# Kernel optimization log

Hardware: AMD Instinct MI355X
Metric: run time of the kernel (lower is better)

The kernel has to match this reference:

```python
import jax, jax.numpy as jnp
import numpy as np

_CLIP_MIN = 1e-06
_POS_ALPHA = 0.001
NUM_CLASSES = 26
RADIUS = 3
POOL = 3  # rmi_pool_size == rmi_pool_stride
HALF_D = RADIUS * RADIUS


def _max_pool2d(x):
    # torch F.max_pool2d(kernel=3, stride=3, padding=1): pads with -inf
    return jax.lax.reduce_window(
        x, -jnp.inf, jax.lax.max,
        window_dimensions=(1, 1, POOL, POOL),
        window_strides=(1, 1, POOL, POOL),
        padding=[(0, 0), (0, 0), (1, 1), (1, 1)])


def _get_pairs(x):
    # stack radius^2 shifted views: [n,c,H,W] -> [n,c,half_d,new_h,new_w]
    h, w = x.shape[2], x.shape[3]
    nh, nw = h - (RADIUS - 1), w - (RADIUS - 1)
    views = [x[:, :, y:y + nh, xx:xx + nw] for y in range(RADIUS) for xx in range(RADIUS)]
    return jnp.stack(views, axis=2)


def _log_det_by_cholesky(m):
    chol = jnp.linalg.cholesky(m)
    diag = jnp.diagonal(chol, axis1=-2, axis2=-1)
    return 2.0 * jnp.sum(jnp.log(diag + 1e-08), axis=-1)


def _rmi_lower_bound(labels_4D, probs_4D):
    labels_4D = _max_pool2d(labels_4D)
    probs_4D = _max_pool2d(probs_4D)
    n, c = labels_4D.shape[0], labels_4D.shape[1]
    la = _get_pairs(labels_4D).reshape(n, c, HALF_D, -1)  # [n,c,9,M]
    pr = _get_pairs(probs_4D).reshape(n, c, HALF_D, -1)
    eye = jnp.eye(HALF_D, dtype=pr.dtype)
    la = la - jnp.mean(la, axis=3, keepdims=True)
    pr = pr - jnp.mean(pr, axis=3, keepdims=True)
    la_cov = jnp.einsum('ncdm,ncem->ncde', la, la)
    pr_cov = jnp.einsum('ncdm,ncem->ncde', pr, pr)
    pr_cov_inv = jnp.linalg.inv(pr_cov + eye * _POS_ALPHA)
    la_pr_cov = jnp.einsum('ncdm,ncem->ncde', la, pr)
    appro_var = la_cov - jnp.einsum('ncde,ncef,ncgf->ncdg', la_pr_cov, pr_cov_inv, la_pr_cov)
    rmi_now = 0.5 * _log_det_by_cholesky(appro_var + eye * _POS_ALPHA)  # [n,c]
    rmi_per_class = jnp.mean(rmi_now.reshape(-1, NUM_CLASSES), axis=0) / float(HALF_D)
    return jnp.sum(rmi_per_class)


def setup_inputs() -> dict:
    key = jax.random.key(0)
    k1, k2, k3 = jax.random.split(key, 3)
    n, c, h, w = 4, NUM_CLASSES, 512, 512
    cls_score = jax.random.normal(k1, (n, c, h, w), dtype=jnp.float32)
    new_targets = jax.random.randint(k2, (n, c, h, w), 0, 2).astype(jnp.float32)
    valid_indices = jax.random.randint(k3, (n, h, w), 0, 2).astype(jnp.float32)
    return {"cls_score": cls_score, "new_targets": new_targets, "valid_indices": valid_indices}


def reference(cls_score, new_targets, valid_indices):
    mask = valid_indices[:, None, :, :]  # [n,1,h,w]
    valid_onehot = new_targets * mask
    probs = jax.nn.sigmoid(cls_score) * mask + _CLIP_MIN
    return _rmi_lower_bound(valid_onehot, probs)
```

## Files before the change

### kernel.cpp

```cpp
#include <hip/hip_runtime.h>
#include <math.h>

#define NUM_CLASSES 26
#define HH 512
#define WW 512
#define NB 4
#define PHH 171
#define PWW 171
#define NHH 169
#define NWW 169
#define MPTS (NHH*NWW)
#define NCT (NB*NUM_CLASSES)
#define CLIPV 1e-6f
#define NCHUNK 8
#define RPC 22
#define NSLOT 189

__global__ __launch_bounds__(256, 3) void fused_kernel(const float* __restrict__ cls,
        const float* __restrict__ tgt, const float* __restrict__ mask,
        float* __restrict__ partial) {
    const int nc = blockIdx.x, ch = blockIdx.y;
    const int n = nc / NUM_CLASSES;
    const int lane = threadIdx.x & 63, wave = threadIdx.x >> 6;
    const int rowbase = ch * RPC;
    const int rc = (rowbase + RPC <= NHH) ? RPC : (NHH - rowbase);
    const int trows = rc + 2;

    __shared__ float tP[24][176];
    __shared__ float tL[24][176];
    __shared__ float amS[4][512];
    __shared__ float lmS[4][512];

    const float4* c4 = (const float4*)(cls  + (size_t)nc * HH * WW);
    const float4* t4 = (const float4*)(tgt  + (size_t)nc * HH * WW);
    const float4* m4 = (const float4*)(mask + (size_t)n  * HH * WW);

    for (int k = 0; k < 6; ++k) {
        int tr = wave + 4 * k;
        if (tr >= trows) break;
        int ph = rowbase + tr;
        float am[8], lm[8];
        #pragma unroll
        for (int j = 0; j < 8; ++j) { am[j] = -INFINITY; lm[j] = 0.f; }
        const int r0 = 3 * ph - 1;
        #pragma unroll
        for (int s = 0; s < 3; ++s) {
            int r = r0 + s;
            r = r < 0 ? 0 : r;
            int rb = r * 128;
            #pragma unroll
            for (int g = 0; g < 2; ++g) {
                int i4 = rb + lane + 64 * g;
                float4 c = c4[i4];
                float4 t = t4[i4];
                float4 m = m4[i4];
                float cc[4] = {c.x, c.y, c.z, c.w};
                float tt[4] = {t.x, t.y, t.z, t.w};
                float mm[4] = {m.x, m.y, m.z, m.w};
                #pragma unroll
                for (int q = 0; q < 4; ++q) {
                    int j = 4 * g + q;
                    am[j] = fmaxf(am[j], mm[q] > 0.5f ? cc[q] : -INFINITY);
                    lm[j] = fmaxf(lm[j], tt[q] * mm[q]);
                }
            }
        }
        *(float4*)&amS[wave][4 * lane]       = make_float4(am[0], am[1], am[2], am[3]);
        *(float4*)&amS[wave][256 + 4 * lane] = make_float4(am[4], am[5], am[6], am[7]);
        *(float4*)&lmS[wave][4 * lane]       = make_float4(lm[0], lm[1], lm[2], lm[3]);
        *(float4*)&lmS[wave][256 + 4 * lane] = make_float4(lm[4], lm[5], lm[6], lm[7]);
        #pragma unroll
        for (int j = 0; j < 3; ++j) {
            int pw = lane + 64 * j;
            if (pw < PWW) {
                int cM = 3 * pw;
                float a = fmaxf(amS[wave][cM], amS[wave][cM + 1]);
                float l = fmaxf(lmS[wave][cM], lmS[wave][cM + 1]);
                if (cM > 0) {
                    a = fmaxf(a, amS[wave][cM - 1]);
                    l = fmaxf(l, lmS[wave][cM - 1]);
                }
                tP[tr][pw] = __fdividef(1.0f, 1.0f + __expf(-a)) + CLIPV;
                tL[tr][pw] = (l > 0.5f) ? 1.0f : 0.0f;
            }
        }
        if (lane < 5) {
            tP[tr][171 + lane] = 0.f;
            tL[tr][171 + lane] = 0.f;
        }
    }
    __syncthreads();

    const int items = rc * 43;
    float* pbase = partial + (size_t)ch * NSLOT * NCT + nc;

    if (wave < 2) {
        const float (*src)[176] = wave ? tP : tL;
        float acc[45], sm[9];
        #pragma unroll
        for (int k = 0; k < 45; ++k) acc[k] = 0.f;
        #pragma unroll
        for (int k = 0; k < 9; ++k) sm[k] = 0.f;

        for (int it = lane; it < items; it += 64) {
            int tr = it / 43;
            int j0 = (it - tr * 43) * 4;
            const float* rp = &src[tr][j0];
            float4 x0 = *(const float4*)(rp);
            float4 x1 = *(const float4*)(rp + 4);
            float4 y0 = *(const float4*)(rp + 176);
            float4 y1 = *(const float4*)(rp + 180);
            float4 z0 = *(const float4*)(rp + 352);
            float4 z1 = *(const float4*)(rp + 356);
            float r0[8] = {x0.x, x0.y, x0.z, x0.w, x1.x, x1.y, x1.z, x1.w};
            float r1[8] = {y0.x, y0.y, y0.z, y0.w, y1.x, y1.y, y1.z, y1.w};
            float r2[8] = {z0.x, z0.y, z0.z, z0.w, z1.x, z1.y, z1.z, z1.w};
            #pragma unroll
            for (int q = 0; q < 4; ++q) {
                float sel = (j0 + q < NWW) ? 1.f : 0.f;
                float v[9], vs[9];
                v[0] = r0[q]; v[1] = r0[q + 1]; v[2] = r0[q + 2];
                v[3] = r1[q]; v[4] = r1[q + 1]; v[5] = r1[q + 2];
                v[6] = r2[q]; v[7] = r2[q + 1]; v[8] = r2[q + 2];
                #pragma unroll
                for (int d = 0; d < 9; ++d) { vs[d] = v[d] * sel; sm[d] += vs[d]; }
                int k = 0;
                #pragma unroll
                for (int d = 0; d < 9; ++d)
                    #pragma unroll
                    for (int e = d; e < 9; ++e)
                        acc[k++] += vs[d] * v[e];
            }
        }
        #pragma unroll
        for (int k = 0; k < 45; ++k) {
            float x = acc[k];
            #pragma unroll
            for (int off = 32; off > 0; off >>= 1) x += __shfl_down(x, off);
            if (lane == 0) pbase[(size_t)((wave == 0 ? 0 : 45) + k) * NCT] = x;
        }
        #pragma unroll
        for (int k = 0; k < 9; ++k) {
            float x = sm[k];
            #pragma unroll
            for (int off = 32; off > 0; off >>= 1) x += __shfl_down(x, off);
            if (lane == 0) pbase[(size_t)((wave == 0 ? 171 : 180) + k) * NCT] = x;
        }
    } else {
        const int nd  = (wave == 2) ? 5 : 4;
        const int dof = (wave == 2) ? 0 : 5;
        float acc[45];
        #pragma unroll
        for (int k = 0; k < 45; ++k) acc[k] = 0.f;

        for (int it = lane; it < items; it += 64) {
            int tr = it / 43;
            int j0 = (it - tr * 43) * 4;
            const float* pp = &tP[tr][j0];
            float4 px0 = *(const float4*)(pp);
            float4 px1 = *(const float4*)(pp + 4);
            float4 py0 = *(const float4*)(pp + 176);
            float4 py1 = *(const float4*)(pp + 180);
            float4 pz0 = *(const float4*)(pp + 352);
            float4 pz1 = *(const float4*)(pp + 356);
            float pr0[8] = {px0.x, px0.y, px0.z, px0.w, px1.x, px1.y, px1.z, px1.w};
            float pr1[8] = {py0.x, py0.y, py0.z, py0.w, py1.x, py1.y, py1.z, py1.w};
            float pr2[8] = {pz0.x, pz0.y, pz0.z, pz0.w, pz1.x, pz1.y, pz1.z, pz1.w};
            const float* la  = &tL[tr + (wave == 2 ? 0 : 1)][j0];
            const float* lb2 = &tL[tr + (wave == 2 ? 1 : 2)][j0];
            float4 la0 = *(const float4*)(la);
            float4 la1 = *(const float4*)(la + 4);
            float4 lb0 = *(const float4*)(lb2);
            float4 lb1 = *(const float4*)(lb2 + 4);
            float lrA[8] = {la0.x, la0.y, la0.z, la0.w, la1.x, la1.y, la1.z, la1.w};
            float lrB[8] = {lb0.x, lb0.y, lb0.z, lb0.w, lb1.x, lb1.y, lb1.z, lb1.w};
            #pragma unroll
            for (int q = 0; q < 4; ++q) {
                float sel = (j0 + q < NWW) ? 1.f : 0.f;
                float vp[9];
                vp[0] = pr0[q]; vp[1] = pr0[q + 1]; vp[2] = pr0[q + 2];
                vp[3] = pr1[q]; vp[4] = pr1[q + 1]; vp[5] = pr1[q + 2];
                vp[6] = pr2[q]; vp[7] = pr2[q + 1]; vp[8] = pr2[q + 2];
                float vl[5];
                if (wave == 2) {
                    vl[0] = lrA[q] * sel; vl[1] = lrA[q + 1] * sel; vl[2] = lrA[q + 2] * sel;
                    vl[3] = lrB[q] * sel; vl[4] = lrB[q + 1] * sel;
                } else {
                    vl[0] = lrA[q + 2] * sel;
                    vl[1] = lrB[q] * sel; vl[2] = lrB[q + 1] * sel; vl[3] = lrB[q + 2] * sel;
                }
                #pragma unroll
                for (int d = 0; d < 5; ++d) {
                    if (d < nd) {
                        #pragma unroll
                        for (int e = 0; e < 9; ++e)
                            acc[d * 9 + e] += vl[d] * vp[e];
                    }
                }
            }
        }
        const int nred = nd * 9;
        #pragma unroll
        for (int k = 0; k < 45; ++k) {
            if (k < nred) {
                float x = acc[k];
                #pragma unroll
                for (int off = 32; off > 0; off >>= 1) x += __shfl_down(x, off);
                if (lane == 0) pbase[(size_t)(90 + dof * 9 + k) * NCT] = x;
            }
        }
    }
}

__global__ __launch_bounds__(128) void solve_kernel(const float* __restrict__ partial,
                                                    double* __restrict__ per_nc) {
    const int nc = blockIdx.x;
    const int tid = threadIdx.x;
    __shared__ double cl[45], cp[45], clp[81], sL[9], sP[9];
    __shared__ double All[81], C[81], Pm[81], X[81], A[81];
    __shared__ double logacc;

    for (int s = tid; s < NSLOT; s += 128) {
        double acc = 0.0;
        for (int ch = 0; ch < NCHUNK; ++ch)
            acc += (double)partial[((size_t)ch * NSLOT + s) * NCT + nc];
        if (s < 45)       cl[s] = acc;
        else if (s < 90)  cp[s - 45] = acc;
        else if (s < 171) clp[s - 90] = acc;
        else if (s < 180) sL[s - 171] = acc;
        else              sP[s - 180] = acc;
    }
    if (tid == 0) logacc = 0.0;
    __syncthreads();

    const double M = (double)MPTS;
    if (tid < 81) {
        int d = tid / 9, e = tid % 9;
        int lo = d < e ? d : e, hi = d < e ? e : d;
        int k = 9 * lo - lo * (lo - 1) / 2 + (hi - lo);
        All[tid] = cl[k] - sL[d] * sL[e] / M;
        C[tid]   = cp[k] - sP[d] * sP[e] / M + (d == e ? 1e-3 : 0.0);
        Pm[tid]  = clp[tid] - sL[d] * sP[e] / M;
    }
    __syncthreads();

    for (int k = 0; k < 9; ++k) {
        if (tid == 0) C[k * 9 + k] = sqrt(fmax(C[k * 9 + k], 1e-30));
        __syncthreads();
        if (tid > k && tid < 9) C[tid * 9 + k] /= C[k * 9 + k];
        __syncthreads();
        if (tid < 81) {
            int i = tid / 9, j = tid % 9;
            if (j > k && i >= j) C[i * 9 + j] -= C[i * 9 + k] * C[j * 9 + k];
        }
        __syncthreads();
    }

    for (int e = 0; e < 9; ++e) {
        if (tid < 9) {
            int d = tid;
            double sum = Pm[d * 9 + e];
            for (int k = 0; k < e; ++k) sum -= C[e * 9 + k] * X[k * 9 + d];
            X[e * 9 + d] = sum / C[e * 9 + e];
        }
        __syncthreads();
    }

    if (tid < 81) {
        int d = tid / 9, g = tid % 9;
        double w = 0.0;
        #pragma unroll
        for (int e = 0; e < 9; ++e) w += X[e * 9 + d] * X[e * 9 + g];
        A[tid] = All[tid] - w + (d == g ? 1e-3 : 0.0);
    }
    __syncthreads();

    for (int k = 0; k < 9; ++k) {
        if (tid == 0) {
            double piv = sqrt(fmax(A[k * 9 + k], 0.0));
            A[k * 9 + k] = piv;
            logacc += log(piv + 1e-8);
        }
        __syncthreads();
        if (tid > k && tid < 9) A[tid * 9 + k] /= A[k * 9 + k];
        __syncthreads();
        if (tid < 81) {
            int i = tid / 9, j = tid % 9;
            if (j > k && i >= j) A[i * 9 + j] -= A[i * 9 + k] * A[j * 9 + k];
        }
        __syncthreads();
    }
    if (tid == 0) per_nc[nc] = logacc;
}

__global__ __launch_bounds__(128) void reduce_kernel(const double* __restrict__ per_nc,
                                                     float* __restrict__ out) {
    int t = threadIdx.x;
    double r = (t < NCT) ? per_nc[t] : 0.0;
    __shared__ double red[128];
    red[t] = r;
    __syncthreads();
    for (int s = 64; s > 0; s >>= 1) {
        if (t < s) red[t] += red[t + s];
        __syncthreads();
    }
    if (t == 0) out[0] = (float)(red[0] / 36.0);
}

extern "C" void kernel_launch(void* const* d_in, const int* in_sizes, int n_in,
                              void* d_out, int out_size, void* d_ws, size_t ws_size,
                              hipStream_t stream) {
    const float* cls  = (const float*)d_in[0];
    const float* tgt  = (const float*)d_in[1];
    const float* mask = (const float*)d_in[2];

    double* per_nc  = (double*)d_ws;
    float*  partial = (float*)(per_nc + 128);

    dim3 gfused(NCT, NCHUNK);
    fused_kernel<<<gfused, 256, 0, stream>>>(cls, tgt, mask, partial);

    solve_kernel<<<NCT, 128, 0, stream>>>(partial, per_nc);

    reduce_kernel<<<1, 128, 0, stream>>>(per_nc, (float*)d_out);
}
```

Baseline: 278.0 us.

## Split fused kernel column-wise into two halves to double grid and shrink LDS

```diff
diff --git a/kernel.cpp b/kernel.cpp
--- a/kernel.cpp
+++ b/kernel.cpp
@@ -15,21 +15,29 @@
 #define NCHUNK 8
 #define RPC 22
 #define NSLOT 189
-
-__global__ __launch_bounds__(256, 3) void fused_kernel(const float* __restrict__ cls,
+#define NSLICE (NCHUNK*2)
+#define TW 96
+#define NQ 22
+
+__global__ __launch_bounds__(256, 5) void fused_kernel(const float* __restrict__ cls,
         const float* __restrict__ tgt, const float* __restrict__ mask,
         float* __restrict__ partial) {
-    const int nc = blockIdx.x, ch = blockIdx.y;
+    const int nc = blockIdx.x, ch = blockIdx.y, half = blockIdx.z;
     const int n = nc / NUM_CLASSES;
     const int lane = threadIdx.x & 63, wave = threadIdx.x >> 6;
     const int rowbase = ch * RPC;
     const int rc = (rowbase + RPC <= NHH) ? RPC : (NHH - rowbase);
     const int trows = rc + 2;
 
-    __shared__ float tP[24][176];
-    __shared__ float tL[24][176];
-    __shared__ float amS[4][512];
-    __shared__ float lmS[4][512];
+    const int ibase4 = half ? 65 : 0;
+    const int nf4    = half ? 63 : 72;
+    const int ioff   = half ? 260 : 0;
+    const int cbase  = half ? 88 : 0;
+
+    __shared__ float tP[24][TW];
+    __shared__ float tL[24][TW];
+    __shared__ float amS[4][288];
+    __shared__ float lmS[4][288];
 
     const float4* c4 = (const float4*)(cls  + (size_t)nc * HH * WW);
     const float4* t4 = (const float4*)(tgt  + (size_t)nc * HH * WW);
@@ -50,52 +58,61 @@
             int rb = r * 128;
             #pragma unroll
             for (int g = 0; g < 2; ++g) {
-                int i4 = rb + lane + 64 * g;
-                float4 c = c4[i4];
-                float4 t = t4[i4];
-                float4 m = m4[i4];
-                float cc[4] = {c.x, c.y, c.z, c.w};
-                float tt[4] = {t.x, t.y, t.z, t.w};
-                float mm[4] = {m.x, m.y, m.z, m.w};
-                #pragma unroll
-                for (int q = 0; q < 4; ++q) {
-                    int j = 4 * g + q;
-                    am[j] = fmaxf(am[j], mm[q] > 0.5f ? cc[q] : -INFINITY);
-                    lm[j] = fmaxf(lm[j], tt[q] * mm[q]);
+                int idx = 64 * g + lane;
+                if (idx < nf4) {
+                    int i4 = rb + ibase4 + idx;
+                    float4 c = c4[i4];
+                    float4 t = t4[i4];
+                    float4 m = m4[i4];
+                    float cc[4] = {c.x, c.y, c.z, c.w};
+                    float tt[4] = {t.x, t.y, t.z, t.w};
+                    float mm[4] = {m.x, m.y, m.z, m.w};
+                    #pragma unroll
+                    for (int q = 0; q < 4; ++q) {
+                        int j = 4 * g + q;
+                        am[j] = fmaxf(am[j], mm[q] > 0.5f ? cc[q] : -INFINITY);
+                        lm[j] = fmaxf(lm[j], tt[q] * mm[q]);
+                    }
                 }
             }
         }
-        *(float4*)&amS[wave][4 * lane]       = make_float4(am[0], am[1], am[2], am[3]);
-        *(float4*)&amS[wave][256 + 4 * lane] = make_float4(am[4], am[5], am[6], am[7]);
-        *(float4*)&lmS[wave][4 * lane]       = make_float4(lm[0], lm[1], lm[2], lm[3]);
-        *(float4*)&lmS[wave][256 + 4 * lane] = make_float4(lm[4], lm[5], lm[6], lm[7]);
-        #pragma unroll
-        for (int j = 0; j < 3; ++j) {
-            int pw = lane + 64 * j;
-            if (pw < PWW) {
-                int cM = 3 * pw;
-                float a = fmaxf(amS[wave][cM], amS[wave][cM + 1]);
-                float l = fmaxf(lmS[wave][cM], lmS[wave][cM + 1]);
-                if (cM > 0) {
-                    a = fmaxf(a, amS[wave][cM - 1]);
-                    l = fmaxf(l, lmS[wave][cM - 1]);
+        if (lane < nf4)
+        {
+            *(float4*)&amS[wave][4 * lane] = make_float4(am[0], am[1], am[2], am[3]);
+            *(float4*)&lmS[wave][4 * lane] = make_float4(lm[0], lm[1], lm[2], lm[3]);
+        }
+        if (64 + lane < nf4) {
+            *(float4*)&amS[wave][256 + 4 * lane] = make_float4(am[4], am[5], am[6], am[7]);
+            *(float4*)&lmS[wave][256 + 4 * lane] = make_float4(lm[4], lm[5], lm[6], lm[7]);
+        }
+        #pragma unroll
+        for (int j = 0; j < 2; ++j) {
+            int tc = lane + 64 * j;
+            if (tc >= TW) continue;
+            int gc = cbase + tc;
+            if (gc < PWW) {
+                int base = 3 * gc - 1 - ioff;
+                float a = fmaxf(amS[wave][base + 1], amS[wave][base + 2]);
+                float l = fmaxf(lmS[wave][base + 1], lmS[wave][base + 2]);
+                if (base >= 0) {
+                    a = fmaxf(a, amS[wave][base]);
+                    l = fmaxf(l, lmS[wave][base]);
                 }
-                tP[tr][pw] = __fdividef(1.0f, 1.0f + __expf(-a)) + CLIPV;
-                tL[tr][pw] = (l > 0.5f) ? 1.0f : 0.0f;
-            }
-        }
-        if (lane < 5) {
-            tP[tr][171 + lane] = 0.f;
-            tL[tr][171 + lane] = 0.f;
-        }
-    }
-    __syncthreads();
-
-    const int items = rc * 43;
-    float* pbase = partial + (size_t)ch * NSLOT * NCT + nc;
+                tP[tr][tc] = __fdividef(1.0f, 1.0f + __expf(-a)) + CLIPV;
+                tL[tr][tc] = (l > 0.5f) ? 1.0f : 0.0f;
+            } else {
+                tP[tr][tc] = 0.f;
+                tL[tr][tc] = 0.f;
+            }
+        }
+    }
+    __syncthreads();
+
+    const int items = rc * NQ;
+    float* pbase = partial + (size_t)(ch * 2 + half) * NSLOT * NCT + nc;
 
     if (wave < 2) {
-        const float (*src)[176] = wave ? tP : tL;
+        const float (*src)[TW] = wave ? tP : tL;
         float acc[45], sm[9];
         #pragma unroll
         for (int k = 0; k < 45; ++k) acc[k] = 0.f;
@@ -103,21 +120,22 @@
         for (int k = 0; k < 9; ++k) sm[k] = 0.f;
 
         for (int it = lane; it < items; it += 64) {
-            int tr = it / 43;
-            int j0 = (it - tr * 43) * 4;
-            const float* rp = &src[tr][j0];
+            int tr  = it / NQ;
+            int j0l = (it - tr * NQ) * 4;
+            const float* rp = &src[tr][j0l];
             float4 x0 = *(const float4*)(rp);
             float4 x1 = *(const float4*)(rp + 4);
-            float4 y0 = *(const float4*)(rp + 176);
-            float4 y1 = *(const float4*)(rp + 180);
-            float4 z0 = *(const float4*)(rp + 352);
-            float4 z1 = *(const float4*)(rp + 356);
+            float4 y0 = *(const float4*)(rp + TW);
+            float4 y1 = *(const float4*)(rp + TW + 4);
+            float4 z0 = *(const float4*)(rp + 2 * TW);
+            float4 z1 = *(const float4*)(rp + 2 * TW + 4);
             float r0[8] = {x0.x, x0.y, x0.z, x0.w, x1.x, x1.y, x1.z, x1.w};
             float r1[8] = {y0.x, y0.y, y0.z, y0.w, y1.x, y1.y, y1.z, y1.w};
             float r2[8] = {z0.x, z0.y, z0.z, z0.w, z1.x, z1.y, z1.z, z1.w};
+            int jg = cbase + j0l;
             #pragma unroll
             for (int q = 0; q < 4; ++q) {
-                float sel = (j0 + q < NWW) ? 1.f : 0.f;
+                float sel = (jg + q < NWW) ? 1.f : 0.f;
                 float v[9], vs[9];
                 v[0] = r0[q]; v[1] = r0[q + 1]; v[2] = r0[q + 2];
                 v[3] = r1[q]; v[4] = r1[q + 1]; v[5] = r1[q + 2];
@@ -154,29 +172,30 @@
         for (int k = 0; k < 45; ++k) acc[k] = 0.f;
 
         for (int it = lane; it < items; it += 64) {
-            int tr = it / 43;
-            int j0 = (it - tr * 43) * 4;
-            const float* pp = &tP[tr][j0];
+            int tr  = it / NQ;
+            int j0l = (it - tr * NQ) * 4;
+            const float* pp = &tP[tr][j0l];
             float4 px0 = *(const float4*)(pp);
             float4 px1 = *(const float4*)(pp + 4);
-            float4 py0 = *(const float4*)(pp + 176);
-            float4 py1 = *(const float4*)(pp + 180);
-            float4 pz0 = *(const float4*)(pp + 352);
-            float4 pz1 = *(const float4*)(pp + 356);
+            float4 py0 = *(const float4*)(pp + TW);
+            float4 py1 = *(const float4*)(pp + TW + 4);
+            float4 pz0 = *(const float4*)(pp + 2 * TW);
+            float4 pz1 = *(const float4*)(pp + 2 * TW + 4);
             float pr0[8] = {px0.x, px0.y, px0.z, px0.w, px1.x, px1.y, px1.z, px1.w};
             float pr1[8] = {py0.x, py0.y, py0.z, py0.w, py1.x, py1.y, py1.z, py1.w};
             float pr2[8] = {pz0.x, pz0.y, pz0.z, pz0.w, pz1.x, pz1.y, pz1.z, pz1.w};
-            const float* la  = &tL[tr + (wave == 2 ? 0 : 1)][j0];
-            const float* lb2 = &tL[tr + (wave == 2 ? 1 : 2)][j0];
+            const float* la  = &tL[tr + (wave == 2 ? 0 : 1)][j0l];
+            const float* lb2 = &tL[tr + (wave == 2 ? 1 : 2)][j0l];
             float4 la0 = *(const float4*)(la);
             float4 la1 = *(const float4*)(la + 4);
             float4 lb0 = *(const float4*)(lb2);
             float4 lb1 = *(const float4*)(lb2 + 4);
             float lrA[8] = {la0.x, la0.y, la0.z, la0.w, la1.x, la1.y, la1.z, la1.w};
             float lrB[8] = {lb0.x, lb0.y, lb0.z, lb0.w, lb1.x, lb1.y, lb1.z, lb1.w};
+            int jg = cbase + j0l;
             #pragma unroll
             for (int q = 0; q < 4; ++q) {
-                float sel = (j0 + q < NWW) ? 1.f : 0.f;
+                float sel = (jg + q < NWW) ? 1.f : 0.f;
                 float vp[9];
                 vp[0] = pr0[q]; vp[1] = pr0[q + 1]; vp[2] = pr0[q + 2];
                 vp[3] = pr1[q]; vp[4] = pr1[q + 1]; vp[5] = pr1[q + 2];
@@ -222,8 +241,8 @@
 
     for (int s = tid; s < NSLOT; s += 128) {
         double acc = 0.0;
-        for (int ch = 0; ch < NCHUNK; ++ch)
-            acc += (double)partial[((size_t)ch * NSLOT + s) * NCT + nc];
+        for (int sl = 0; sl < NSLICE; ++sl)
+            acc += (double)partial[((size_t)sl * NSLOT + s) * NCT + nc];
         if (s < 45)       cl[s] = acc;
         else if (s < 90)  cp[s - 45] = acc;
         else if (s < 171) clp[s - 90] = acc;
@@ -317,7 +336,7 @@
     double* per_nc  = (double*)d_ws;
     float*  partial = (float*)(per_nc + 128);
 
-    dim3 gfused(NCT, NCHUNK);
+    dim3 gfused(NCT, NCHUNK, 2);
     fused_kernel<<<gfused, 256, 0, stream>>>(cls, tgt, mask, partial);
 
     solve_kernel<<<NCT, 128, 0, stream>>>(partial, per_nc);
```

Measured after the change: 494.6 us. 77.9% more time.

## Pool columns in registers with lane shuffles and split rows into more chunks

Applied to the files above, without the earlier changes.

```diff
diff --git a/kernel.cpp b/kernel.cpp
--- a/kernel.cpp
+++ b/kernel.cpp
@@ -12,33 +12,33 @@
 #define MPTS (NHH*NWW)
 #define NCT (NB*NUM_CLASSES)
 #define CLIPV 1e-6f
-#define NCHUNK 8
-#define RPC 22
+#define NCHUNK 13
+#define RPC 13
+#define TROWS 15
+#define TW 180
+#define NQ 43
 #define NSLOT 189
 
-__global__ __launch_bounds__(256, 3) void fused_kernel(const float* __restrict__ cls,
+__global__ __launch_bounds__(256, 4) void fused_kernel(const float* __restrict__ cls,
         const float* __restrict__ tgt, const float* __restrict__ mask,
         float* __restrict__ partial) {
     const int nc = blockIdx.x, ch = blockIdx.y;
     const int n = nc / NUM_CLASSES;
     const int lane = threadIdx.x & 63, wave = threadIdx.x >> 6;
     const int rowbase = ch * RPC;
-    const int rc = (rowbase + RPC <= NHH) ? RPC : (NHH - rowbase);
-    const int trows = rc + 2;
-
-    __shared__ float tP[24][176];
-    __shared__ float tL[24][176];
-    __shared__ float amS[4][512];
-    __shared__ float lmS[4][512];
+
+    __shared__ float tP[TROWS][TW];
+    __shared__ float tL[TROWS][TW];
 
     const float4* c4 = (const float4*)(cls  + (size_t)nc * HH * WW);
     const float4* t4 = (const float4*)(tgt  + (size_t)nc * HH * WW);
     const float4* m4 = (const float4*)(mask + (size_t)n  * HH * WW);
 
-    for (int k = 0; k < 6; ++k) {
-        int tr = wave + 4 * k;
-        if (tr >= trows) break;
-        int ph = rowbase + tr;
+    const int mdiv = lane / 3;
+    const int r3   = lane - 3 * mdiv;
+
+    for (int tr = wave; tr < TROWS; tr += 4) {
+        const int ph = rowbase + tr;
         float am[8], lm[8];
         #pragma unroll
         for (int j = 0; j < 8; ++j) { am[j] = -INFINITY; lm[j] = 0.f; }
@@ -47,55 +47,63 @@
         for (int s = 0; s < 3; ++s) {
             int r = r0 + s;
             r = r < 0 ? 0 : r;
-            int rb = r * 128;
-            #pragma unroll
-            for (int g = 0; g < 2; ++g) {
-                int i4 = rb + lane + 64 * g;
-                float4 c = c4[i4];
-                float4 t = t4[i4];
-                float4 m = m4[i4];
-                float cc[4] = {c.x, c.y, c.z, c.w};
-                float tt[4] = {t.x, t.y, t.z, t.w};
-                float mm[4] = {m.x, m.y, m.z, m.w};
-                #pragma unroll
-                for (int q = 0; q < 4; ++q) {
-                    int j = 4 * g + q;
-                    am[j] = fmaxf(am[j], mm[q] > 0.5f ? cc[q] : -INFINITY);
-                    lm[j] = fmaxf(lm[j], tt[q] * mm[q]);
-                }
-            }
-        }
-        *(float4*)&amS[wave][4 * lane]       = make_float4(am[0], am[1], am[2], am[3]);
-        *(float4*)&amS[wave][256 + 4 * lane] = make_float4(am[4], am[5], am[6], am[7]);
-        *(float4*)&lmS[wave][4 * lane]       = make_float4(lm[0], lm[1], lm[2], lm[3]);
-        *(float4*)&lmS[wave][256 + 4 * lane] = make_float4(lm[4], lm[5], lm[6], lm[7]);
-        #pragma unroll
-        for (int j = 0; j < 3; ++j) {
-            int pw = lane + 64 * j;
-            if (pw < PWW) {
-                int cM = 3 * pw;
-                float a = fmaxf(amS[wave][cM], amS[wave][cM + 1]);
-                float l = fmaxf(lmS[wave][cM], lmS[wave][cM + 1]);
-                if (cM > 0) {
-                    a = fmaxf(a, amS[wave][cM - 1]);
-                    l = fmaxf(l, lmS[wave][cM - 1]);
-                }
-                tP[tr][pw] = __fdividef(1.0f, 1.0f + __expf(-a)) + CLIPV;
-                tL[tr][pw] = (l > 0.5f) ? 1.0f : 0.0f;
-            }
-        }
-        if (lane < 5) {
+            const float4* rc = c4 + r * 128;
+            const float4* rt = t4 + r * 128;
+            const float4* rm = m4 + r * 128;
+            float4 c0 = rc[2 * lane], c1 = rc[2 * lane + 1];
+            float4 t0 = rt[2 * lane], t1 = rt[2 * lane + 1];
+            float4 m0 = rm[2 * lane], m1 = rm[2 * lane + 1];
+            float cc[8] = {c0.x, c0.y, c0.z, c0.w, c1.x, c1.y, c1.z, c1.w};
+            float tt[8] = {t0.x, t0.y, t0.z, t0.w, t1.x, t1.y, t1.z, t1.w};
+            float mm[8] = {m0.x, m0.y, m0.z, m0.w, m1.x, m1.y, m1.z, m1.w};
+            #pragma unroll
+            for (int j = 0; j < 8; ++j) {
+                am[j] = fmaxf(am[j], mm[j] > 0.5f ? cc[j] : -INFINITY);
+                lm[j] = fmaxf(lm[j], tt[j] * mm[j]);
+            }
+        }
+        float am8 = __shfl_down(am[0], 1), am9 = __shfl_down(am[1], 1);
+        float lm8 = __shfl_down(lm[0], 1), lm9 = __shfl_down(lm[1], 1);
+
+        #define EMIT(p, A, B, Cc, LA, LB, LC) { \
+            float a_ = fmaxf(fmaxf(A, B), Cc); \
+            float l_ = fmaxf(fmaxf(LA, LB), LC); \
+            tP[tr][p] = __fdividef(1.0f, 1.0f + __expf(-a_)) + CLIPV; \
+            tL[tr][p] = (l_ > 0.5f) ? 1.0f : 0.0f; }
+        if (r3 == 0) {
+            int p = 8 * mdiv + 1;
+            EMIT(p,     am[2], am[3], am[4], lm[2], lm[3], lm[4]);
+            EMIT(p + 1, am[5], am[6], am[7], lm[5], lm[6], lm[7]);
+            if (lane == 0) {
+                float a_ = fmaxf(am[0], am[1]);
+                float l_ = fmaxf(lm[0], lm[1]);
+                tP[tr][0] = __fdividef(1.0f, 1.0f + __expf(-a_)) + CLIPV;
+                tL[tr][0] = (l_ > 0.5f) ? 1.0f : 0.0f;
+            }
+        } else if (r3 == 1) {
+            int p = 8 * mdiv + 3;
+            EMIT(p,     am[0], am[1], am[2], lm[0], lm[1], lm[2]);
+            EMIT(p + 1, am[3], am[4], am[5], lm[3], lm[4], lm[5]);
+            EMIT(p + 2, am[6], am[7], am8,  lm[6], lm[7], lm8);
+        } else {
+            int p = 8 * mdiv + 6;
+            EMIT(p,     am[1], am[2], am[3], lm[1], lm[2], lm[3]);
+            EMIT(p + 1, am[4], am[5], am[6], lm[4], lm[5], lm[6]);
+            EMIT(p + 2, am[7], am8,  am9,   lm[7], lm8,  lm9);
+        }
+        #undef EMIT
+        if (lane < 9) {
             tP[tr][171 + lane] = 0.f;
             tL[tr][171 + lane] = 0.f;
         }
     }
     __syncthreads();
 
-    const int items = rc * 43;
+    const int items = RPC * NQ;
     float* pbase = partial + (size_t)ch * NSLOT * NCT + nc;
 
     if (wave < 2) {
-        const float (*src)[176] = wave ? tP : tL;
+        const float (*src)[TW] = wave ? tP : tL;
         float acc[45], sm[9];
         #pragma unroll
         for (int k = 0; k < 45; ++k) acc[k] = 0.f;
@@ -103,15 +111,15 @@
         for (int k = 0; k < 9; ++k) sm[k] = 0.f;
 
         for (int it = lane; it < items; it += 64) {
-            int tr = it / 43;
-            int j0 = (it - tr * 43) * 4;
+            int tr = it / NQ;
+            int j0 = (it - tr * NQ) * 4;
             const float* rp = &src[tr][j0];
             float4 x0 = *(const float4*)(rp);
             float4 x1 = *(const float4*)(rp + 4);
-            float4 y0 = *(const float4*)(rp + 176);
-            float4 y1 = *(const float4*)(rp + 180);
-            float4 z0 = *(const float4*)(rp + 352);
-            float4 z1 = *(const float4*)(rp + 356);
+            float4 y0 = *(const float4*)(rp + TW);
+            float4 y1 = *(const float4*)(rp + TW + 4);
+            float4 z0 = *(const float4*)(rp + 2 * TW);
+            float4 z1 = *(const float4*)(rp + 2 * TW + 4);
             float r0[8] = {x0.x, x0.y, x0.z, x0.w, x1.x, x1.y, x1.z, x1.w};
             float r1[8] = {y0.x, y0.y, y0.z, y0.w, y1.x, y1.y, y1.z, y1.w};
             float r2[8] = {z0.x, z0.y, z0.z, z0.w, z1.x, z1.y, z1.z, z1.w};
@@ -154,15 +162,15 @@
         for (int k = 0; k < 45; ++k) acc[k] = 0.f;
 
         for (int it = lane; it < items; it += 64) {
-            int tr = it / 43;
-            int j0 = (it - tr * 43) * 4;
+            int tr = it / NQ;
+            int j0 = (it - tr * NQ) * 4;
             const float* pp = &tP[tr][j0];
             float4 px0 = *(const float4*)(pp);
             float4 px1 = *(const float4*)(pp + 4);
-            float4 py0 = *(const float4*)(pp + 176);
-            float4 py1 = *(const float4*)(pp + 180);
-            float4 pz0 = *(const float4*)(pp + 352);
-            float4 pz1 = *(const float4*)(pp + 356);
+            float4 py0 = *(const float4*)(pp + TW);
+            float4 py1 = *(const float4*)(pp + TW + 4);
+            float4 pz0 = *(const float4*)(pp + 2 * TW);
+            float4 pz1 = *(const float4*)(pp + 2 * TW + 4);
             float pr0[8] = {px0.x, px0.y, px0.z, px0.w, px1.x, px1.y, px1.z, px1.w};
             float pr1[8] = {py0.x, py0.y, py0.z, py0.w, py1.x, py1.y, py1.z, py1.w};
             float pr2[8] = {pz0.x, pz0.y, pz0.z, pz0.w, pz1.x, pz1.y, pz1.z, pz1.w};
@@ -222,8 +230,8 @@
 
     for (int s = tid; s < NSLOT; s += 128) {
         double acc = 0.0;
-        for (int ch = 0; ch < NCHUNK; ++ch)
-            acc += (double)partial[((size_t)ch * NSLOT + s) * NCT + nc];
+        for (int sl = 0; sl < NCHUNK; ++sl)
+            acc += (double)partial[((size_t)sl * NSLOT + s) * NCT + nc];
         if (s < 45)       cl[s] = acc;
         else if (s < 90)  cp[s - 45] = acc;
         else if (s < 171) clp[s - 90] = acc;
```

New measurement: 294.5 us. 5.9% more time.
